# Optimization experiments

Measured on AMD Instinct MI355X. Metric: run time of the kernel, lower is better.

The kernel has to match this reference:

```python
import jax, jax.numpy as jnp
import numpy as np

CASCADING_LOSS = 0.85


def _bilinear_sample(img, px, py):
    """grid_sample(align_corners=True, padding_mode='zeros') in pixel coords.
    img: [B,C,H,W]; px,py: [B,H,W] absolute pixel coordinates."""
    B, C, H, W = img.shape
    x0 = jnp.floor(px)
    y0 = jnp.floor(py)
    x1 = x0 + 1.0
    y1 = y0 + 1.0
    wx1 = px - x0
    wx0 = 1.0 - wx1
    wy1 = py - y0
    wy0 = 1.0 - wy1

    def gather(yi, xi):
        valid = (xi >= 0) & (xi <= W - 1) & (yi >= 0) & (yi <= H - 1)
        xc = jnp.clip(xi, 0, W - 1).astype(jnp.int32)
        yc = jnp.clip(yi, 0, H - 1).astype(jnp.int32)
        # per-batch advanced indexing: [B,C,H,W]
        vals = jax.vmap(lambda im, yy, xx: im[:, yy, xx])(img, yc, xc)
        return vals * valid[:, None, :, :].astype(img.dtype)

    out = (gather(y0, x0) * (wy0 * wx0)[:, None, :, :]
           + gather(y0, x1) * (wy0 * wx1)[:, None, :, :]
           + gather(y1, x0) * (wy1 * wx0)[:, None, :, :]
           + gather(y1, x1) * (wy1 * wx1)[:, None, :, :])
    return out


def _add_flow(img, flw):
    # img: [B,C,H,W]; flw: [B,2,H,W] with channel 0 -> y offset, channel 1 -> x offset
    B, C, H, W = img.shape
    base_x = jnp.arange(W, dtype=img.dtype)[None, None, :]   # [1,1,W]
    base_y = jnp.arange(H, dtype=img.dtype)[None, :, None]   # [1,H,1]
    px = base_x + flw[:, 1, :, :]
    py = base_y + flw[:, 0, :, :]
    return _bilinear_sample(img, px, py)


def _compute_psnr(target, estim):
    mse = jnp.mean((target - estim) ** 2)
    return 10.0 * jnp.log(1.0 / mse) / jnp.log(jnp.asarray(10.0, target.dtype))


def setup_inputs() -> dict:
    key = jax.random.key(0)
    k1, k2, k3 = jax.random.split(key, 3)
    ITERS, B, H, W, C = 12, 4, 384, 512, 3
    flow_tup = jax.random.normal(k1, (ITERS, B, 2, H, W), dtype=jnp.float32)
    frame1 = jax.random.uniform(k2, (B, C, H, W), dtype=jnp.float32)
    frame2 = jax.random.uniform(k3, (B, C, H, W), dtype=jnp.float32)
    return {"flow_tup": flow_tup, "frame1": frame1, "frame2": frame2}


def reference(flow_tup, frame1, frame2):
    n_iters = flow_tup.shape[0]
    # vectorize warp over GRU iterations
    estims = jax.vmap(lambda f: _add_flow(frame1, f))(flow_tup)  # [I,B,C,H,W]
    psnrs = jax.vmap(lambda e: _compute_psnr(frame2, e))(estims)  # [I]
    weights = CASCADING_LOSS ** (n_iters - jnp.arange(n_iters, dtype=flow_tup.dtype))
    loss = -jnp.sum(psnrs * weights)
    return loss
```

## Files before the change

### kernel.cpp

```cpp
#include <hip/hip_runtime.h>
#include <math.h>

#define ITERS 12
#define BATCH 4
#define CH 3
#define H 384
#define W 512

constexpr int HW  = H * W;
constexpr int CHW = CH * HW;
constexpr int TILE_X = 32, TILE_Y = 8;
constexpr int TX_N = W / TILE_X;
constexpr int TY_N = H / TILE_Y;
constexpr int NBLK = BATCH * TX_N * TY_N;
constexpr int HALO_X = 16, HALO_Y = 12;
constexpr int WIN_W = 64;
constexpr int WIN_H = 36;
constexpr int WIN_CH = WIN_H * WIN_W;
constexpr int FSTRIDE = BATCH * 2 * HW;

__global__ __launch_bounds__(256, 4) void warp_mse_kernel(
    const float* __restrict__ flow,
    const float* __restrict__ f1,
    const float* __restrict__ f2,
    float* __restrict__ partials)
{
    __shared__ float win[CH * WIN_CH];
    __shared__ float warp_sums[ITERS][4];

    int tid = threadIdx.x;
    int bx  = blockIdx.x;
    int b   = bx / (TX_N * TY_N);
    int t   = bx - b * (TX_N * TY_N);
    int ty  = t / TX_N;
    int tx  = t - ty * TX_N;
    int x_t = tx * TILE_X, y_t = ty * TILE_Y;

    const float* f1b = f1 + b * CHW;
    const float* f2b = f2 + b * CHW;

    {
        int col = tid & 63;
        int rb  = tid >> 6;
        int gx  = min(max(x_t - HALO_X + col, 0), W - 1);
#pragma unroll
        for (int ch = 0; ch < CH; ++ch) {
#pragma unroll
            for (int k = 0; k < 9; ++k) {
                int row = rb + 4 * k;
                int gy  = min(max(y_t - HALO_Y + row, 0), H - 1);
                win[ch * WIN_CH + row * WIN_W + col] = f1b[ch * HW + gy * W + gx];
            }
        }
    }
    __syncthreads();

    int x = x_t + (tid & 31);
    int y = y_t + (tid >> 5);
    int p = y * W + x;
    float xf = (float)x, yf = (float)y;
    int lane = tid & 63;
    int wid  = tid >> 6;

    float t0 = f2b[p];
    float t1 = f2b[HW + p];
    float t2 = f2b[2 * HW + p];

    const float* fp = flow + b * 2 * HW + p;
    float fy = fp[0];
    float fx = fp[HW];

#pragma unroll 2
    for (int it = 0; it < ITERS; ++it) {
        const float* fpn = fp + FSTRIDE;
        float nfy = 0.0f, nfx = 0.0f;
        if (it + 1 < ITERS) { nfy = fpn[0]; nfx = fpn[HW]; }

        float px = xf + fx;
        float py = yf + fy;
        float x0f = floorf(px), y0f = floorf(py);
        float wx1 = px - x0f, wy1 = py - y0f;
        float wx0 = 1.0f - wx1, wy0 = 1.0f - wy1;
        int x0 = (int)x0f, y0 = (int)y0f;
        int x1 = x0 + 1,  y1 = y0 + 1;

        bool vx0 = (x0 >= 0) & (x0 <= W - 1);
        bool vx1 = (x1 >= 0) & (x1 <= W - 1);
        bool vy0 = (y0 >= 0) & (y0 <= H - 1);
        bool vy1 = (y1 >= 0) & (y1 <= H - 1);

        float w00 = wy0 * wx0 * (float)(vy0 && vx0);
        float w01 = wy0 * wx1 * (float)(vy0 && vx1);
        float w10 = wy1 * wx0 * (float)(vy1 && vx0);
        float w11 = wy1 * wx1 * (float)(vy1 && vx1);

        int lx0 = x0 - (x_t - HALO_X);
        int ly0 = y0 - (y_t - HALO_Y);
        int a   = ly0 * WIN_W + lx0;
        a = min(max(a, 0), WIN_CH - WIN_W - 2);

        float acc = 0.0f;
#pragma unroll
        for (int c = 0; c < CH; ++c) {
            const float* wc = win + c * WIN_CH + a;
            float v = fmaf(w00, wc[0], fmaf(w01, wc[1],
                      fmaf(w10, wc[WIN_W], w11 * wc[WIN_W + 1])));
            float tt = (c == 0) ? t0 : (c == 1) ? t1 : t2;
            float d = tt - v;
            acc = fmaf(d, d, acc);
        }

#pragma unroll
        for (int off = 32; off > 0; off >>= 1)
            acc += __shfl_down(acc, off, 64);
        if (lane == 0) warp_sums[it][wid] = acc;

        fy = nfy; fx = nfx; fp = fpn;
    }

    __syncthreads();
    if (tid < ITERS) {
        int it = tid;
        float s = warp_sums[it][0] + warp_sums[it][1]
                + warp_sums[it][2] + warp_sums[it][3];
        partials[it * NBLK + bx] = s;
    }
}

__global__ __launch_bounds__(768) void finalize_kernel(
    const float* __restrict__ partials,
    float* __restrict__ out)
{
    __shared__ float psnr_w[ITERS];
    int wave = threadIdx.x >> 6;
    int lane = threadIdx.x & 63;

    float s = 0.0f;
    const float* pp = partials + wave * NBLK;
    for (int j = lane; j < NBLK; j += 64)
        s += pp[j];
#pragma unroll
    for (int off = 32; off > 0; off >>= 1)
        s += __shfl_down(s, off, 64);

    if (lane == 0) {
        float mse  = s * (1.0f / (float)(BATCH * CH * HW));
        float psnr = -10.0f * 0.30102999566398f * log2f(mse);
        float w = 1.0f;
        for (int k = 0; k < ITERS - wave; ++k) w *= 0.85f;
        psnr_w[wave] = psnr * w;
    }
    __syncthreads();
    if (threadIdx.x == 0) {
        float loss = 0.0f;
#pragma unroll
        for (int i = 0; i < ITERS; ++i) loss += psnr_w[i];
        out[0] = -loss;
    }
}

extern "C" void kernel_launch(void* const* d_in, const int* in_sizes, int n_in,
                              void* d_out, int out_size, void* d_ws, size_t ws_size,
                              hipStream_t stream) {
    const float* flow = (const float*)d_in[0];
    const float* f1   = (const float*)d_in[1];
    const float* f2   = (const float*)d_in[2];
    float* out        = (float*)d_out;
    float* partials   = (float*)d_ws;

    warp_mse_kernel<<<NBLK, 256, 0, stream>>>(flow, f1, f2, partials);
    finalize_kernel<<<1, 768, 0, stream>>>(partials, out);
}
```

Measured before the change: 154.0 us.

## Process two pixels per thread with larger tiles and deferred per-iteration reduction

Doubles the tile height so each thread handles two horizontally adjacent pixels, loading flow and target values as float2. Per-iteration sums are kept in a 12-entry register array and reduced once at the end through shared memory instead of doing a wavefront shuffle reduction on every iteration. This halves the block count, cuts halo reloading per pixel, and removes 12 shuffle reductions per thread. In exchange register pressure rises and there are fewer blocks to keep the GPU occupied.

```diff
diff --git a/kernel.cpp b/kernel.cpp
--- a/kernel.cpp
+++ b/kernel.cpp
@@ -9,13 +9,13 @@
 
 constexpr int HW  = H * W;
 constexpr int CHW = CH * HW;
-constexpr int TILE_X = 32, TILE_Y = 8;
+constexpr int TILE_X = 32, TILE_Y = 16;
 constexpr int TX_N = W / TILE_X;
 constexpr int TY_N = H / TILE_Y;
 constexpr int NBLK = BATCH * TX_N * TY_N;
 constexpr int HALO_X = 16, HALO_Y = 12;
 constexpr int WIN_W = 64;
-constexpr int WIN_H = 36;
+constexpr int WIN_H = 40;
 constexpr int WIN_CH = WIN_H * WIN_W;
 constexpr int FSTRIDE = BATCH * 2 * HW;
 
@@ -26,7 +26,6 @@
     float* __restrict__ partials)
 {
     __shared__ float win[CH * WIN_CH];
-    __shared__ float warp_sums[ITERS][4];
 
     int tid = threadIdx.x;
     int bx  = blockIdx.x;
@@ -46,7 +45,7 @@
 #pragma unroll
         for (int ch = 0; ch < CH; ++ch) {
 #pragma unroll
-            for (int k = 0; k < 9; ++k) {
+            for (int k = 0; k < WIN_H / 4; ++k) {
                 int row = rb + 4 * k;
                 int gy  = min(max(y_t - HALO_Y + row, 0), H - 1);
                 win[ch * WIN_CH + row * WIN_W + col] = f1b[ch * HW + gy * W + gx];
@@ -55,75 +54,99 @@
     }
     __syncthreads();
 
-    int x = x_t + (tid & 31);
-    int y = y_t + (tid >> 5);
+    int x = x_t + 2 * (tid & 15);
+    int y = y_t + (tid >> 4);
     int p = y * W + x;
-    float xf = (float)x, yf = (float)y;
-    int lane = tid & 63;
-    int wid  = tid >> 6;
+    float yf = (float)y;
 
-    float t0 = f2b[p];
-    float t1 = f2b[HW + p];
-    float t2 = f2b[2 * HW + p];
+    float2 tc0 = *(const float2*)(f2b + p);
+    float2 tc1 = *(const float2*)(f2b + HW + p);
+    float2 tc2 = *(const float2*)(f2b + 2 * HW + p);
+
+    alignas(16) float acc[ITERS];
+#pragma unroll
+    for (int k = 0; k < ITERS; ++k) acc[k] = 0.0f;
 
     const float* fp = flow + b * 2 * HW + p;
-    float fy = fp[0];
-    float fx = fp[HW];
+    float2 fyv = *(const float2*)(fp);
+    float2 fxv = *(const float2*)(fp + HW);
 
-#pragma unroll 2
+#pragma unroll
     for (int it = 0; it < ITERS; ++it) {
         const float* fpn = fp + FSTRIDE;
-        float nfy = 0.0f, nfx = 0.0f;
-        if (it + 1 < ITERS) { nfy = fpn[0]; nfx = fpn[HW]; }
+        float2 nfy = make_float2(0.0f, 0.0f), nfx = make_float2(0.0f, 0.0f);
+        if (it + 1 < ITERS) { nfy = *(const float2*)(fpn); nfx = *(const float2*)(fpn + HW); }
 
-        float px = xf + fx;
-        float py = yf + fy;
-        float x0f = floorf(px), y0f = floorf(py);
-        float wx1 = px - x0f, wy1 = py - y0f;
-        float wx0 = 1.0f - wx1, wy0 = 1.0f - wy1;
-        int x0 = (int)x0f, y0 = (int)y0f;
-        int x1 = x0 + 1,  y1 = y0 + 1;
+        float a_it = 0.0f;
+#pragma unroll
+        for (int j = 0; j < 2; ++j) {
+            float fy = j ? fyv.y : fyv.x;
+            float fx = j ? fxv.y : fxv.x;
+            float pxf = (float)(x + j) + fx;
+            float pyf = yf + fy;
+            float x0f = floorf(pxf), y0f = floorf(pyf);
+            float wx1 = pxf - x0f, wy1 = pyf - y0f;
+            float wx0 = 1.0f - wx1, wy0 = 1.0f - wy1;
+            int x0 = (int)x0f, y0 = (int)y0f;
+            int x1 = x0 + 1,  y1 = y0 + 1;
 
-        bool vx0 = (x0 >= 0) & (x0 <= W - 1);
-        bool vx1 = (x1 >= 0) & (x1 <= W - 1);
-        bool vy0 = (y0 >= 0) & (y0 <= H - 1);
-        bool vy1 = (y1 >= 0) & (y1 <= H - 1);
+            bool vx0 = (x0 >= 0) & (x0 <= W - 1);
+            bool vx1 = (x1 >= 0) & (x1 <= W - 1);
+            bool vy0 = (y0 >= 0) & (y0 <= H - 1);
+            bool vy1 = (y1 >= 0) & (y1 <= H - 1);
 
-        float w00 = wy0 * wx0 * (float)(vy0 && vx0);
-        float w01 = wy0 * wx1 * (float)(vy0 && vx1);
-        float w10 = wy1 * wx0 * (float)(vy1 && vx0);
-        float w11 = wy1 * wx1 * (float)(vy1 && vx1);
+            float w00 = wy0 * wx0 * (float)(vy0 && vx0);
+            float w01 = wy0 * wx1 * (float)(vy0 && vx1);
+            float w10 = wy1 * wx0 * (float)(vy1 && vx0);
+            float w11 = wy1 * wx1 * (float)(vy1 && vx1);
 
-        int lx0 = x0 - (x_t - HALO_X);
-        int ly0 = y0 - (y_t - HALO_Y);
-        int a   = ly0 * WIN_W + lx0;
-        a = min(max(a, 0), WIN_CH - WIN_W - 2);
+            int lx0 = x0 - (x_t - HALO_X);
+            int ly0 = y0 - (y_t - HALO_Y);
+            int a   = ly0 * WIN_W + lx0;
+            a = min(max(a, 0), WIN_CH - WIN_W - 2);
 
-        float acc = 0.0f;
-#pragma unroll
-        for (int c = 0; c < CH; ++c) {
-            const float* wc = win + c * WIN_CH + a;
-            float v = fmaf(w00, wc[0], fmaf(w01, wc[1],
-                      fmaf(w10, wc[WIN_W], w11 * wc[WIN_W + 1])));
-            float tt = (c == 0) ? t0 : (c == 1) ? t1 : t2;
-            float d = tt - v;
-            acc = fmaf(d, d, acc);
+            float t0 = j ? tc0.y : tc0.x;
+            float t1 = j ? tc1.y : tc1.x;
+            float t2 = j ? tc2.y : tc2.x;
+
+            const float* w0 = win + a;
+            const float* w1 = win + WIN_CH + a;
+            const float* w2 = win + 2 * WIN_CH + a;
+            float v0 = fmaf(w00, w0[0], fmaf(w01, w0[1],
+                       fmaf(w10, w0[WIN_W], w11 * w0[WIN_W + 1])));
+            float v1 = fmaf(w00, w1[0], fmaf(w01, w1[1],
+                       fmaf(w10, w1[WIN_W], w11 * w1[WIN_W + 1])));
+            float v2 = fmaf(w00, w2[0], fmaf(w01, w2[1],
+                       fmaf(w10, w2[WIN_W], w11 * w2[WIN_W + 1])));
+
+            float d0 = t0 - v0, d1 = t1 - v1, d2 = t2 - v2;
+            a_it += fmaf(d0, d0, fmaf(d1, d1, d2 * d2));
         }
-
-#pragma unroll
-        for (int off = 32; off > 0; off >>= 1)
-            acc += __shfl_down(acc, off, 64);
-        if (lane == 0) warp_sums[it][wid] = acc;
-
-        fy = nfy; fx = nfx; fp = fpn;
+        acc[it] = a_it;
+        fyv = nfy; fxv = nfx; fp = fpn;
     }
 
     __syncthreads();
-    if (tid < ITERS) {
-        int it = tid;
-        float s = warp_sums[it][0] + warp_sums[it][1]
-                + warp_sums[it][2] + warp_sums[it][3];
-        partials[it * NBLK + bx] = s;
+    float4* sc4 = (float4*)win;
+    const float4* av = (const float4*)acc;
+    sc4[tid * 3 + 0] = av[0];
+    sc4[tid * 3 + 1] = av[1];
+    sc4[tid * 3 + 2] = av[2];
+    __syncthreads();
+
+    int lane = tid & 63;
+    int wv   = tid >> 6;
+#pragma unroll
+    for (int r = 0; r < 3; ++r) {
+        int k = wv + 4 * r;
+        float s = win[lane * 12 + k]
+                + win[(lane + 64) * 12 + k]
+                + win[(lane + 128) * 12 + k]
+                + win[(lane + 192) * 12 + k];
+#pragma unroll
+        for (int off = 32; off > 0; off >>= 1)
+            s += __shfl_down(s, off, 64);
+        if (lane == 0) partials[k * NBLK + bx] = s;
     }
 }
 
```

Measured after the change: 136.4 us. -11.4%, faster.
